# Optimization experiments

Hardware: AMD Instinct MI355X
Metric: run time of the kernel (lower is better)

## Reference

```python
import jax, jax.numpy as jnp
import numpy as np

B = 262144   # batch of polygon pairs
N = 8        # vertices per polygon
TWO_PI = 2.0 * np.pi


def sort_poly(p):
    # sort vertices CCW by angle about the centroid (repo's sort_poly)
    c = jnp.mean(p, axis=-2, keepdims=True)
    v = p - c
    ang = jnp.arctan2(v[..., 1], v[..., 0])
    order = jnp.argsort(ang, axis=-1)
    return jnp.take_along_axis(p, order[..., None], axis=-2)


def shoelace(p):
    # signed area, positive for CCW polygons: [..., K, 2] -> [...]
    q = jnp.roll(p, -1, axis=-2)
    return 0.5 * jnp.sum(p[..., 0] * q[..., 1] - p[..., 1] * q[..., 0], axis=-1)


def points_inside(pts, poly):
    # pts [B,K,2], poly [B,N,2] convex CCW -> bool [B,K]
    a = poly[:, None, :, :]
    e = jnp.roll(poly, -1, axis=1)[:, None, :, :] - a
    w = pts[:, :, None, :] - a
    cr = e[..., 0] * w[..., 1] - e[..., 1] * w[..., 0]
    return jnp.all(cr >= -1e-6, axis=-1)


def edge_intersections(pa, pb):
    # all pairwise edge-edge intersection points: -> pts [B,N*N,2], ok [B,N*N]
    bsz, n, _ = pa.shape
    p1 = pa[:, :, None, :]
    d1 = jnp.roll(pa, -1, axis=1)[:, :, None, :] - p1
    q1 = pb[:, None, :, :]
    d2 = jnp.roll(pb, -1, axis=1)[:, None, :, :] - q1
    denom = d1[..., 0] * d2[..., 1] - d1[..., 1] * d2[..., 0]
    safe = jnp.where(jnp.abs(denom) < 1e-9, 1.0, denom)
    r = q1 - p1
    t = (r[..., 0] * d2[..., 1] - r[..., 1] * d2[..., 0]) / safe
    u = (r[..., 0] * d1[..., 1] - r[..., 1] * d1[..., 0]) / safe
    ok = (jnp.abs(denom) >= 1e-9) & (t >= 0.0) & (t <= 1.0) & (u >= 0.0) & (u <= 1.0)
    pts = p1 + t[..., None] * d1
    return pts.reshape(bsz, n * n, 2), ok.reshape(bsz, n * n)


def convex_intersection_area(pa, pb):
    # intersection of two convex CCW polygons: candidate vertices are
    # (a-verts inside b) + (b-verts inside a) + edge-edge intersections,
    # sorted by angle around their centroid, shoelace with masked padding.
    ia = points_inside(pa, pb)
    ib = points_inside(pb, pa)
    xpts, xok = edge_intersections(pa, pb)
    cand = jnp.concatenate([pa, pb, xpts], axis=1)          # [B, 2N+N^2, 2]
    mask = jnp.concatenate([ia, ib, xok], axis=1)
    cnt = jnp.sum(mask, axis=1)
    mf = mask[..., None].astype(cand.dtype)
    ctr = jnp.sum(cand * mf, axis=1) / jnp.maximum(cnt, 1).astype(cand.dtype)[..., None]
    v = cand - ctr[:, None, :]
    ang = jnp.where(mask, jnp.arctan2(v[..., 1], v[..., 0]), 1e9)  # invalid -> end
    order = jnp.argsort(ang, axis=1)
    cand = jnp.take_along_axis(cand, order[..., None], axis=1)
    mask = jnp.take_along_axis(mask, order, axis=1)
    cand = jnp.where(mask[..., None], cand, cand[:, 0:1, :])  # pad w/ first valid pt
    area = shoelace(cand)
    return jnp.where(cnt >= 3, jnp.maximum(area, 0.0), 0.0)


def hull_area_single(pts):
    # gift wrapping (Jarvis march) over M points, accumulating CCW shoelace sum
    m = pts.shape[0]
    start = jnp.lexsort((pts[:, 0], pts[:, 1]))[0]  # lowest y, tie-break lowest x

    def step(carry, _):
        cur, d, done, acc = carry
        cp = pts[cur]
        v = pts - cp
        dist2 = jnp.sum(v * v, axis=-1)
        ang = jnp.arctan2(d[0] * v[:, 1] - d[1] * v[:, 0],
                          d[0] * v[:, 0] + d[1] * v[:, 1])
        ang = jnp.where(dist2 < 1e-16, jnp.inf, jnp.mod(ang, TWO_PI))
        nxt = jnp.argmin(ang)
        npnt = pts[nxt]
        acc = acc + jnp.where(done, 0.0, cp[0] * npnt[1] - cp[1] * npnt[0])
        done = done | (nxt == start)
        return (nxt, npnt - cp, done, acc), None

    init = (start, jnp.array([1.0, 0.0], pts.dtype), jnp.array(False),
            jnp.zeros((), pts.dtype))
    (_, _, _, acc), _ = jax.lax.scan(step, init, None, length=m)
    return 0.5 * acc


def _make_convex(key, bsz, n):
    # random convex polygons: points on random ellipses at sorted angles
    k1, k2, k3, k4 = jax.random.split(key, 4)
    th = jnp.sort(jax.random.uniform(k1, (bsz, n)) * TWO_PI, axis=1)
    rx = 0.5 + 1.5 * jax.random.uniform(k2, (bsz, 1))
    ry = 0.5 + 1.5 * jax.random.uniform(k3, (bsz, 1))
    c = jax.random.uniform(k4, (bsz, 2)) * 2.0 - 1.0
    return c[:, None, :] + jnp.stack([rx * jnp.cos(th), ry * jnp.sin(th)], axis=-1)


def setup_inputs() -> dict:
    key = jax.random.key(0)
    ka, kb = jax.random.split(key)
    a = _make_convex(ka, B, N).astype(jnp.float32)
    b = _make_convex(kb, B, N).astype(jnp.float32)
    return {"a": a, "b": b}


def reference(a, b):
    pa = sort_poly(a)
    pb = sort_poly(b)
    area_a = shoelace(pa)
    area_b = shoelace(pb)
    inter = convex_intersection_area(pa, pb)     # [B]
    union = area_a + area_b - inter              # shapely a.union(b).area
    iou = inter / union
    all_pts = jnp.concatenate([a, b], axis=1)    # [B, 2N, 2]
    ch_area = jax.vmap(hull_area_single)(all_pts)
    ciou = iou - (ch_area - union) / ch_area
    return jnp.mean(ciou)                        # sum over batch / batch_size
```

## Files before the change

### kernel.cpp

```cpp
#include <hip/hip_runtime.h>

#define TPB 256

__global__ __launch_bounds__(TPB, 2) void ciou_main(
    const float* __restrict__ A,
    const float* __restrict__ Bq,
    double* __restrict__ partial,
    int nbatch, int tail)
{
    const int t = threadIdx.x;
    const int i0 = blockIdx.x * TPB + t;
    const bool live = !tail || (i0 < nbatch);
    const int i = live ? i0 : (nbatch - 1);

    float ax0,ax1,ax2,ax3,ax4,ax5,ax6,ax7;
    float ay0,ay1,ay2,ay3,ay4,ay5,ay6,ay7;
    float bx0,bx1,bx2,bx3,bx4,bx5,bx6,bx7;
    float by0,by1,by2,by3,by4,by5,by6,by7;
    {
        const float4* pa = (const float4*)(A + (size_t)i * 16);
        const float4* pb = (const float4*)(Bq + (size_t)i * 16);
        float4 q;
        q = pa[0]; ax0=q.x; ay0=q.y; ax1=q.z; ay1=q.w;
        q = pa[1]; ax2=q.x; ay2=q.y; ax3=q.z; ay3=q.w;
        q = pa[2]; ax4=q.x; ay4=q.y; ax5=q.z; ay5=q.w;
        q = pa[3]; ax6=q.x; ay6=q.y; ax7=q.z; ay7=q.w;
        q = pb[0]; bx0=q.x; by0=q.y; bx1=q.z; by1=q.w;
        q = pb[1]; bx2=q.x; by2=q.y; bx3=q.z; by3=q.w;
        q = pb[2]; bx4=q.x; by4=q.y; bx5=q.z; by5=q.w;
        q = pb[3]; bx6=q.x; by6=q.y; bx7=q.z; by7=q.w;
    }

#define MKEA(I,IN) float eax##I = ax##IN - ax##I, eay##I = ay##IN - ay##I;
#define MKEB(I,IN) float ebx##I = bx##IN - bx##I, eby##I = by##IN - by##I;
    MKEA(0,1) MKEA(1,2) MKEA(2,3) MKEA(3,4)
    MKEA(4,5) MKEA(5,6) MKEA(6,7) MKEA(7,0)
    MKEB(0,1) MKEB(1,2) MKEB(2,3) MKEB(3,4)
    MKEB(4,5) MKEB(5,6) MKEB(6,7) MKEB(7,0)
#define MKCA(I,IN) float ca##I = ax##I*ay##IN - ay##I*ax##IN;
#define MKCB(I,IN) float cb##I = bx##I*by##IN - by##I*bx##IN;
    MKCA(0,1) MKCA(1,2) MKCA(2,3) MKCA(3,4)
    MKCA(4,5) MKCA(5,6) MKCA(6,7) MKCA(7,0)
    MKCB(0,1) MKCB(1,2) MKCB(2,3) MKCB(3,4)
    MKCB(4,5) MKCB(5,6) MKCB(6,7) MKCB(7,0)
    float area_a = 0.5f * (((ca0+ca1)+(ca2+ca3)) + ((ca4+ca5)+(ca6+ca7)));
    float area_b = 0.5f * (((cb0+cb1)+(cb2+cb3)) + ((cb4+cb5)+(cb6+cb7)));

    float inter2 = 0.f;

#define HP(T0,T1,EX,EY,CC) { \
        float aa = EX*Py - EY*Px + (CC); \
        float bb = EX*Dy - EY*Dx; \
        float tc = __fdividef(-aa, bb); \
        float h = bb * 1e38f; \
        T0 = fmaxf(T0, fminf(tc, h)); \
        T1 = fminf(T1, fmaxf(tc, h)); }

#define HPB HP(t0a,t1a, ebx0,eby0,cb0) HP(t0b,t1b, ebx1,eby1,cb1) \
            HP(t0a,t1a, ebx2,eby2,cb2) HP(t0b,t1b, ebx3,eby3,cb3) \
            HP(t0a,t1a, ebx4,eby4,cb4) HP(t0b,t1b, ebx5,eby5,cb5) \
            HP(t0a,t1a, ebx6,eby6,cb6) HP(t0b,t1b, ebx7,eby7,cb7)
#define HPA HP(t0a,t1a, eax0,eay0,ca0) HP(t0b,t1b, eax1,eay1,ca1) \
            HP(t0a,t1a, eax2,eay2,ca2) HP(t0b,t1b, eax3,eay3,ca3) \
            HP(t0a,t1a, eax4,eay4,ca4) HP(t0b,t1b, eax5,eay5,ca5) \
            HP(t0a,t1a, eax6,eay6,ca6) HP(t0b,t1b, eax7,eay7,ca7)

#define EDGE(PX,PY,DX,DY,CPD,HPS) { \
        const float Px = (PX), Py = (PY); \
        const float Dx = (DX), Dy = (DY); \
        float t0a = 0.f, t1a = 1.f, t0b = 0.f, t1b = 1.f; \
        HPS \
        float dt = fminf(t1a, t1b) - fmaxf(t0a, t0b); \
        inter2 += fmaxf(dt, 0.f) * (CPD); }

    EDGE(ax0,ay0, eax0,eay0, ca0, HPB) EDGE(ax1,ay1, eax1,eay1, ca1, HPB)
    EDGE(ax2,ay2, eax2,eay2, ca2, HPB) EDGE(ax3,ay3, eax3,eay3, ca3, HPB)
    EDGE(ax4,ay4, eax4,eay4, ca4, HPB) EDGE(ax5,ay5, eax5,eay5, ca5, HPB)
    EDGE(ax6,ay6, eax6,eay6, ca6, HPB) EDGE(ax7,ay7, eax7,eay7, ca7, HPB)
    EDGE(bx0,by0, ebx0,eby0, cb0, HPA) EDGE(bx1,by1, ebx1,eby1, cb1, HPA)
    EDGE(bx2,by2, ebx2,eby2, cb2, HPA) EDGE(bx3,by3, ebx3,eby3, cb3, HPA)
    EDGE(bx4,by4, ebx4,eby4, cb4, HPA) EDGE(bx5,by5, ebx5,eby5, cb5, HPA)
    EDGE(bx6,by6, ebx6,eby6, cb6, HPA) EDGE(bx7,by7, ebx7,eby7, cb7, HPA)

    float inter = fmaxf(0.5f * inter2, 0.f);
    float uni = area_a + area_b - inter;
    float iou = __fdividef(inter, uni);

#define MIN2(X1,Y1,X2,Y2) { \
        bool bs = ((Y2) < (Y1)) || (((Y2) == (Y1)) && ((X2) < (X1))); \
        X1 = bs ? (X2) : (X1); Y1 = bs ? (Y2) : (Y1); }
    float m0x=ax0, m0y=ay0; MIN2(m0x,m0y, ax1,ay1)
    float m1x=ax2, m1y=ay2; MIN2(m1x,m1y, ax3,ay3)
    float m2x=ax4, m2y=ay4; MIN2(m2x,m2y, ax5,ay5)
    float m3x=ax6, m3y=ay6; MIN2(m3x,m3y, ax7,ay7)
    float m4x=bx0, m4y=by0; MIN2(m4x,m4y, bx1,by1)
    float m5x=bx2, m5y=by2; MIN2(m5x,m5y, bx3,by3)
    float m6x=bx4, m6y=by4; MIN2(m6x,m6y, bx5,by5)
    float m7x=bx6, m7y=by6; MIN2(m7x,m7y, bx7,by7)
    MIN2(m0x,m0y, m1x,m1y) MIN2(m2x,m2y, m3x,m3y)
    MIN2(m4x,m4y, m5x,m5y) MIN2(m6x,m6y, m7x,m7y)
    MIN2(m0x,m0y, m2x,m2y) MIN2(m4x,m4y, m6x,m6y)
    MIN2(m0x,m0y, m4x,m4y)
    const float stx = m0x, sty = m0y;

#define SCANC(CDX,CDY,NX,NY,PX,PY) { \
        float vx = (PX) - cxv, vy = (PY) - cyv; \
        float cr = CDX*vy - CDY*vx; \
        bool take = cr < 0.f; \
        NX = take ? (PX) : NX;  NY = take ? (PY) : NY; \
        CDX = take ? vx : CDX;  CDY = take ? vy : CDY; }
#define MERGE(CDX,CDY,NX,NY,CDX2,CDY2,NX2,NY2) { \
        float cr = CDX*(CDY2) - CDY*(CDX2); \
        bool take = cr < 0.f; \
        NX = take ? (NX2) : NX;  NY = take ? (NY2) : NY; \
        CDX = take ? (CDX2) : CDX; CDY = take ? (CDY2) : CDY; }

    float cxv = stx, cyv = sty, accH = 0.f;
    float pdx = 1.f, pdy = 0.f;
    bool done = false;
#pragma unroll 1
    for (int it = 0; it < 16; ++it) {
        float ndx = -pdx, ndy = -pdy;
        float cdx0 = ndx, cdy0 = ndy, nx0 = cxv, ny0 = cyv;
        float cdx1 = ndx, cdy1 = ndy, nx1 = cxv, ny1 = cyv;
        float cdx2 = ndx, cdy2 = ndy, nx2 = cxv, ny2 = cyv;
        float cdx3 = ndx, cdy3 = ndy, nx3 = cxv, ny3 = cyv;
        float cdx4 = ndx, cdy4 = ndy, nx4 = cxv, ny4 = cyv;
        float cdx5 = ndx, cdy5 = ndy, nx5 = cxv, ny5 = cyv;
        float cdx6 = ndx, cdy6 = ndy, nx6 = cxv, ny6 = cyv;
        float cdx7 = ndx, cdy7 = ndy, nx7 = cxv, ny7 = cyv;
        SCANC(cdx0,cdy0,nx0,ny0, ax0,ay0) SCANC(cdx0,cdy0,nx0,ny0, ax1,ay1)
        SCANC(cdx1,cdy1,nx1,ny1, ax2,ay2) SCANC(cdx1,cdy1,nx1,ny1, ax3,ay3)
        SCANC(cdx2,cdy2,nx2,ny2, ax4,ay4) SCANC(cdx2,cdy2,nx2,ny2, ax5,ay5)
        SCANC(cdx3,cdy3,nx3,ny3, ax6,ay6) SCANC(cdx3,cdy3,nx3,ny3, ax7,ay7)
        SCANC(cdx4,cdy4,nx4,ny4, bx0,by0) SCANC(cdx4,cdy4,nx4,ny4, bx1,by1)
        SCANC(cdx5,cdy5,nx5,ny5, bx2,by2) SCANC(cdx5,cdy5,nx5,ny5, bx3,by3)
        SCANC(cdx6,cdy6,nx6,ny6, bx4,by4) SCANC(cdx6,cdy6,nx6,ny6, bx5,by5)
        SCANC(cdx7,cdy7,nx7,ny7, bx6,by6) SCANC(cdx7,cdy7,nx7,ny7, bx7,by7)
        MERGE(cdx0,cdy0,nx0,ny0, cdx1,cdy1,nx1,ny1)
        MERGE(cdx2,cdy2,nx2,ny2, cdx3,cdy3,nx3,ny3)
        MERGE(cdx4,cdy4,nx4,ny4, cdx5,cdy5,nx5,ny5)
        MERGE(cdx6,cdy6,nx6,ny6, cdx7,cdy7,nx7,ny7)
        MERGE(cdx0,cdy0,nx0,ny0, cdx2,cdy2,nx2,ny2)
        MERGE(cdx4,cdy4,nx4,ny4, cdx6,cdy6,nx6,ny6)
        MERGE(cdx0,cdy0,nx0,ny0, cdx4,cdy4,nx4,ny4)
        accH += done ? 0.f : (cxv*ny0 - cyv*nx0);
        done = done || (nx0 == stx && ny0 == sty);
        pdx = cdx0; pdy = cdy0;
        cxv = nx0; cyv = ny0;
        if (__all(done)) break;
    }
    float ch = 0.5f * accH;

    float val = iou - __fdividef(ch - uni, ch);
    float v = live ? val : 0.f;

    #pragma unroll
    for (int off = 32; off > 0; off >>= 1) v += __shfl_down(v, off);
    __shared__ float wsum[4];
    int lane = t & 63, wid = t >> 6;
    if (lane == 0) wsum[wid] = v;
    __syncthreads();
    if (t == 0) {
        partial[blockIdx.x] = (double)wsum[0] + (double)wsum[1]
                            + (double)wsum[2] + (double)wsum[3];
    }
}

__global__ __launch_bounds__(256) void ciou_finalize(
    const double* __restrict__ partial, float* __restrict__ out,
    int nparts, int nbatch)
{
    double v = 0.0;
    for (int j = threadIdx.x; j < nparts; j += 256) v += partial[j];
    #pragma unroll
    for (int off = 32; off > 0; off >>= 1) v += __shfl_down(v, off);
    __shared__ double s[4];
    int lane = threadIdx.x & 63, wid = threadIdx.x >> 6;
    if (lane == 0) s[wid] = v;
    __syncthreads();
    if (threadIdx.x == 0)
        out[0] = (float)((s[0] + s[1] + s[2] + s[3]) / (double)nbatch);
}

extern "C" void kernel_launch(void* const* d_in, const int* in_sizes, int n_in,
                              void* d_out, int out_size, void* d_ws, size_t ws_size,
                              hipStream_t stream) {
    const float* a = (const float*)d_in[0];
    const float* b = (const float*)d_in[1];
    float* out = (float*)d_out;
    int nbatch = in_sizes[0] / 16;
    int nblocks = (nbatch + TPB - 1) / TPB;
    int tail = (nblocks * TPB != nbatch) ? 1 : 0;
    double* partial = (double*)d_ws;
    ciou_main<<<nblocks, TPB, 0, stream>>>(a, b, partial, nbatch, tail);
    ciou_finalize<<<1, 256, 0, stream>>>(partial, out, nblocks, nbatch);
}
```

Before: 100.1 us.

## Compute convex hull area via edge masks and bridge tangents instead of gift-wrapping

Replaces the iterative gift-wrapping hull walk (up to 16 data-dependent iterations, each scanning 16 points) with a closed-form hull area. Edges of each polygon that lie outside the other are marked by masks set inside the existing half-plane tests. The bridge edges between A and B vertices are found with a fixed 64-pair tangent test that accumulates signed cross products. This removes the loop, the wave-level vote and its divergence, at the cost of about 64 fixed bridge evaluations per pair and a dependence on strict convexity and the CCW vertex order for correctness.

```diff
diff --git a/kernel.cpp b/kernel.cpp
--- a/kernel.cpp
+++ b/kernel.cpp
@@ -47,23 +47,26 @@
     float area_b = 0.5f * (((cb0+cb1)+(cb2+cb3)) + ((cb4+cb5)+(cb6+cb7)));
 
     float inter2 = 0.f;
+    float mb0=1.f,mb1=1.f,mb2=1.f,mb3=1.f,mb4=1.f,mb5=1.f,mb6=1.f,mb7=1.f;
+    float ma0=1.f,ma1=1.f,ma2=1.f,ma3=1.f,ma4=1.f,ma5=1.f,ma6=1.f,ma7=1.f;
 
-#define HP(T0,T1,EX,EY,CC) { \
+#define HP(T0,T1,EX,EY,CC,MK) { \
         float aa = EX*Py - EY*Px + (CC); \
         float bb = EX*Dy - EY*Dx; \
+        MK = (aa >= 0.f) ? MK : 0.f; \
         float tc = __fdividef(-aa, bb); \
         float h = bb * 1e38f; \
         T0 = fmaxf(T0, fminf(tc, h)); \
         T1 = fminf(T1, fmaxf(tc, h)); }
 
-#define HPB HP(t0a,t1a, ebx0,eby0,cb0) HP(t0b,t1b, ebx1,eby1,cb1) \
-            HP(t0a,t1a, ebx2,eby2,cb2) HP(t0b,t1b, ebx3,eby3,cb3) \
-            HP(t0a,t1a, ebx4,eby4,cb4) HP(t0b,t1b, ebx5,eby5,cb5) \
-            HP(t0a,t1a, ebx6,eby6,cb6) HP(t0b,t1b, ebx7,eby7,cb7)
-#define HPA HP(t0a,t1a, eax0,eay0,ca0) HP(t0b,t1b, eax1,eay1,ca1) \
-            HP(t0a,t1a, eax2,eay2,ca2) HP(t0b,t1b, eax3,eay3,ca3) \
-            HP(t0a,t1a, eax4,eay4,ca4) HP(t0b,t1b, eax5,eay5,ca5) \
-            HP(t0a,t1a, eax6,eay6,ca6) HP(t0b,t1b, eax7,eay7,ca7)
+#define HPB HP(t0a,t1a, ebx0,eby0,cb0,mb0) HP(t0b,t1b, ebx1,eby1,cb1,mb1) \
+            HP(t0a,t1a, ebx2,eby2,cb2,mb2) HP(t0b,t1b, ebx3,eby3,cb3,mb3) \
+            HP(t0a,t1a, ebx4,eby4,cb4,mb4) HP(t0b,t1b, ebx5,eby5,cb5,mb5) \
+            HP(t0a,t1a, ebx6,eby6,cb6,mb6) HP(t0b,t1b, ebx7,eby7,cb7,mb7)
+#define HPA HP(t0a,t1a, eax0,eay0,ca0,ma0) HP(t0b,t1b, eax1,eay1,ca1,ma1) \
+            HP(t0a,t1a, eax2,eay2,ca2,ma2) HP(t0b,t1b, eax3,eay3,ca3,ma3) \
+            HP(t0a,t1a, eax4,eay4,ca4,ma4) HP(t0b,t1b, eax5,eay5,ca5,ma5) \
+            HP(t0a,t1a, eax6,eay6,ca6,ma6) HP(t0b,t1b, eax7,eay7,ca7,ma7)
 
 #define EDGE(PX,PY,DX,DY,CPD,HPS) { \
         const float Px = (PX), Py = (PY); \
@@ -86,71 +89,44 @@
     float uni = area_a + area_b - inter;
     float iou = __fdividef(inter, uni);
 
-#define MIN2(X1,Y1,X2,Y2) { \
-        bool bs = ((Y2) < (Y1)) || (((Y2) == (Y1)) && ((X2) < (X1))); \
-        X1 = bs ? (X2) : (X1); Y1 = bs ? (Y2) : (Y1); }
-    float m0x=ax0, m0y=ay0; MIN2(m0x,m0y, ax1,ay1)
-    float m1x=ax2, m1y=ay2; MIN2(m1x,m1y, ax3,ay3)
-    float m2x=ax4, m2y=ay4; MIN2(m2x,m2y, ax5,ay5)
-    float m3x=ax6, m3y=ay6; MIN2(m3x,m3y, ax7,ay7)
-    float m4x=bx0, m4y=by0; MIN2(m4x,m4y, bx1,by1)
-    float m5x=bx2, m5y=by2; MIN2(m5x,m5y, bx3,by3)
-    float m6x=bx4, m6y=by4; MIN2(m6x,m6y, bx5,by5)
-    float m7x=bx6, m7y=by6; MIN2(m7x,m7y, bx7,by7)
-    MIN2(m0x,m0y, m1x,m1y) MIN2(m2x,m2y, m3x,m3y)
-    MIN2(m4x,m4y, m5x,m5y) MIN2(m6x,m6y, m7x,m7y)
-    MIN2(m0x,m0y, m2x,m2y) MIN2(m4x,m4y, m6x,m6y)
-    MIN2(m0x,m0y, m4x,m4y)
-    const float stx = m0x, sty = m0y;
+    float eS = ((ca0*ma0 + ca1*ma1) + (ca2*ma2 + ca3*ma3))
+             + ((ca4*ma4 + ca5*ma5) + (ca6*ma6 + ca7*ma7))
+             + ((cb0*mb0 + cb1*mb1) + (cb2*mb2 + cb3*mb3))
+             + ((cb4*mb4 + cb5*mb5) + (cb6*mb6 + cb7*mb7));
 
-#define SCANC(CDX,CDY,NX,NY,PX,PY) { \
-        float vx = (PX) - cxv, vy = (PY) - cyv; \
-        float cr = CDX*vy - CDY*vx; \
-        bool take = cr < 0.f; \
-        NX = take ? (PX) : NX;  NY = take ? (PY) : NY; \
-        CDX = take ? vx : CDX;  CDY = take ? vy : CDY; }
-#define MERGE(CDX,CDY,NX,NY,CDX2,CDY2,NX2,NY2) { \
-        float cr = CDX*(CDY2) - CDY*(CDX2); \
-        bool take = cr < 0.f; \
-        NX = take ? (NX2) : NX;  NY = take ? (NY2) : NY; \
-        CDX = take ? (CDX2) : CDX; CDY = take ? (CDY2) : CDY; }
+    float hb0 = 0.f, hb1 = 0.f, hb2 = 0.f, hb3 = 0.f;
+#define BR(AXI,AYI,EAXI,EAYI,EAXP,EAYP, BXJ,BYJ,EBXJ,EBYJ,EBXP,EBYP, ACC) { \
+        float Dx = (BXJ)-(AXI), Dy = (BYJ)-(AYI); \
+        float c1 = Dx*(EAYI) - Dy*(EAXI); \
+        float c2 = Dx*(EAYP) - Dy*(EAXP); \
+        float c3 = Dx*(EBYJ) - Dy*(EBXJ); \
+        float c4 = Dx*(EBYP) - Dy*(EBXP); \
+        float cx = (AXI)*(BYJ) - (AYI)*(BXJ); \
+        bool ab = (c1 >= 0.f) & (c2 <= 0.f) & (c3 >= 0.f) & (c4 <= 0.f); \
+        bool ba = (c1 <= 0.f) & (c2 >= 0.f) & (c3 <= 0.f) & (c4 >= 0.f); \
+        float sgn = (ab ? 1.f : 0.f) - (ba ? 1.f : 0.f); \
+        ACC = fmaf(sgn, cx, ACC); }
 
-    float cxv = stx, cyv = sty, accH = 0.f;
-    float pdx = 1.f, pdy = 0.f;
-    bool done = false;
-#pragma unroll 1
-    for (int it = 0; it < 16; ++it) {
-        float ndx = -pdx, ndy = -pdy;
-        float cdx0 = ndx, cdy0 = ndy, nx0 = cxv, ny0 = cyv;
-        float cdx1 = ndx, cdy1 = ndy, nx1 = cxv, ny1 = cyv;
-        float cdx2 = ndx, cdy2 = ndy, nx2 = cxv, ny2 = cyv;
-        float cdx3 = ndx, cdy3 = ndy, nx3 = cxv, ny3 = cyv;
-        float cdx4 = ndx, cdy4 = ndy, nx4 = cxv, ny4 = cyv;
-        float cdx5 = ndx, cdy5 = ndy, nx5 = cxv, ny5 = cyv;
-        float cdx6 = ndx, cdy6 = ndy, nx6 = cxv, ny6 = cyv;
-        float cdx7 = ndx, cdy7 = ndy, nx7 = cxv, ny7 = cyv;
-        SCANC(cdx0,cdy0,nx0,ny0, ax0,ay0) SCANC(cdx0,cdy0,nx0,ny0, ax1,ay1)
-        SCANC(cdx1,cdy1,nx1,ny1, ax2,ay2) SCANC(cdx1,cdy1,nx1,ny1, ax3,ay3)
-        SCANC(cdx2,cdy2,nx2,ny2, ax4,ay4) SCANC(cdx2,cdy2,nx2,ny2, ax5,ay5)
-        SCANC(cdx3,cdy3,nx3,ny3, ax6,ay6) SCANC(cdx3,cdy3,nx3,ny3, ax7,ay7)
-        SCANC(cdx4,cdy4,nx4,ny4, bx0,by0) SCANC(cdx4,cdy4,nx4,ny4, bx1,by1)
-        SCANC(cdx5,cdy5,nx5,ny5, bx2,by2) SCANC(cdx5,cdy5,nx5,ny5, bx3,by3)
-        SCANC(cdx6,cdy6,nx6,ny6, bx4,by4) SCANC(cdx6,cdy6,nx6,ny6, bx5,by5)
-        SCANC(cdx7,cdy7,nx7,ny7, bx6,by6) SCANC(cdx7,cdy7,nx7,ny7, bx7,by7)
-        MERGE(cdx0,cdy0,nx0,ny0, cdx1,cdy1,nx1,ny1)
-        MERGE(cdx2,cdy2,nx2,ny2, cdx3,cdy3,nx3,ny3)
-        MERGE(cdx4,cdy4,nx4,ny4, cdx5,cdy5,nx5,ny5)
-        MERGE(cdx6,cdy6,nx6,ny6, cdx7,cdy7,nx7,ny7)
-        MERGE(cdx0,cdy0,nx0,ny0, cdx2,cdy2,nx2,ny2)
-        MERGE(cdx4,cdy4,nx4,ny4, cdx6,cdy6,nx6,ny6)
-        MERGE(cdx0,cdy0,nx0,ny0, cdx4,cdy4,nx4,ny4)
-        accH += done ? 0.f : (cxv*ny0 - cyv*nx0);
-        done = done || (nx0 == stx && ny0 == sty);
-        pdx = cdx0; pdy = cdy0;
-        cxv = nx0; cyv = ny0;
-        if (__all(done)) break;
-    }
-    float ch = 0.5f * accH;
+#define BRROW(AXI,AYI,EAXI,EAYI,EAXP,EAYP) \
+    BR(AXI,AYI,EAXI,EAYI,EAXP,EAYP, bx0,by0, ebx0,eby0, ebx7,eby7, hb0) \
+    BR(AXI,AYI,EAXI,EAYI,EAXP,EAYP, bx1,by1, ebx1,eby1, ebx0,eby0, hb1) \
+    BR(AXI,AYI,EAXI,EAYI,EAXP,EAYP, bx2,by2, ebx2,eby2, ebx1,eby1, hb2) \
+    BR(AXI,AYI,EAXI,EAYI,EAXP,EAYP, bx3,by3, ebx3,eby3, ebx2,eby2, hb3) \
+    BR(AXI,AYI,EAXI,EAYI,EAXP,EAYP, bx4,by4, ebx4,eby4, ebx3,eby3, hb0) \
+    BR(AXI,AYI,EAXI,EAYI,EAXP,EAYP, bx5,by5, ebx5,eby5, ebx4,eby4, hb1) \
+    BR(AXI,AYI,EAXI,EAYI,EAXP,EAYP, bx6,by6, ebx6,eby6, ebx5,eby5, hb2) \
+    BR(AXI,AYI,EAXI,EAYI,EAXP,EAYP, bx7,by7, ebx7,eby7, ebx6,eby6, hb3)
+
+    BRROW(ax0,ay0, eax0,eay0, eax7,eay7)
+    BRROW(ax1,ay1, eax1,eay1, eax0,eay0)
+    BRROW(ax2,ay2, eax2,eay2, eax1,eay1)
+    BRROW(ax3,ay3, eax3,eay3, eax2,eay2)
+    BRROW(ax4,ay4, eax4,eay4, eax3,eay3)
+    BRROW(ax5,ay5, eax5,eay5, eax4,eay4)
+    BRROW(ax6,ay6, eax6,eay6, eax5,eay5)
+    BRROW(ax7,ay7, eax7,eay7, eax6,eay6)
+
+    float ch = 0.5f * (eS + ((hb0 + hb1) + (hb2 + hb3)));
 
     float val = iou - __fdividef(ch - uni, ch);
     float v = live ? val : 0.f;
```

After: 143.1 us. 1.43x slower.
